# Performance work log

Hardware: AMD Instinct MI355X
Metric: run time of the kernel (lower is better)

The kernel has to match this reference:

```python
import jax, jax.numpy as jnp
import numpy as np

B, S, D = 4, 2048, 1024
H = 16
HD = D // H  # 64
SCALE = HD ** 0.5
LN_EPS = 1e-5


def setup_inputs() -> dict:
    key = jax.random.key(0)
    ks = jax.random.split(key, 13)
    std = 1.0 / np.sqrt(D)
    inp = {
        'q': jax.random.normal(ks[0], (B, S, D), jnp.float32),
        'k': jax.random.normal(ks[1], (B, S, D), jnp.float32),
        'v': jax.random.normal(ks[2], (B, S, D), jnp.float32),
        'Wq': jax.random.normal(ks[3], (D, D), jnp.float32) * std,
        'bq': jnp.zeros((D,), jnp.float32),
        'Wk': jax.random.normal(ks[4], (D, D), jnp.float32) * std,
        'bk': jnp.zeros((D,), jnp.float32),
        'Wv': jax.random.normal(ks[5], (D, D), jnp.float32) * std,
        'bv': jnp.zeros((D,), jnp.float32),
        'Wp': jax.random.normal(ks[6], (D, D), jnp.float32) * std,
        'bp': jnp.zeros((D,), jnp.float32),
        'gamma': jnp.ones((D,), jnp.float32),
        'beta': jnp.zeros((D,), jnp.float32),
    }
    return inp


def reference(q, k, v, Wq, bq, Wk, bk, Wv, bv, Wp, bp, gamma, beta):
    res = q
    # QKV projections, split into heads: [B, S, H, HD]
    qh = (q @ Wq + bq).reshape(B, S, H, HD)
    kh = (k @ Wk + bk).reshape(B, S, H, HD)
    vh = (v @ Wv + bv).reshape(B, S, H, HD)
    # Full attention scores [B, H, Sq, Sk]
    scores = jnp.einsum('bqhd,bkhd->bhqk', qh, kh) / SCALE
    # Multiplicative causal mask (zeros, NOT -inf) applied post-scale
    tril = jnp.tril(jnp.ones((S, S), scores.dtype))
    scores = scores * tril
    attn = jax.nn.softmax(scores, axis=-1)
    ctx = jnp.einsum('bhqk,bkhd->bqhd', attn, vh).reshape(B, S, D)
    out = ctx @ Wp + bp + res
    # LayerNorm over last dim
    mu = out.mean(-1, keepdims=True)
    var = out.var(-1, keepdims=True)
    return (out - mu) / jnp.sqrt(var + LN_EPS) * gamma + beta
```

## Files before the change

kernel.cpp:

```cpp
#include <hip/hip_runtime.h>

#define B_  4
#define S_  2048
#define D_  1024
#define H_  16
#define HD_ 64

#define ATT_EM 3.35462627903e-4f
#define ATT_C1 0.18033688011f
#define ATT_C0 -11.5415603281f

using v8bf = __attribute__((ext_vector_type(8))) __bf16;
using v8us = __attribute__((ext_vector_type(8))) unsigned short;
using v4f  = __attribute__((ext_vector_type(4))) float;

__device__ inline float bf2f(unsigned short u) {
    union { unsigned int i; float f; } x; x.i = ((unsigned int)u) << 16; return x.f;
}
__device__ inline unsigned short f2bf(float f) {
    union { float f; unsigned int i; } x; x.f = f;
    unsigned int r = x.i + 0x7fffu + ((x.i >> 16) & 1u);
    return (unsigned short)(r >> 16);
}
__device__ inline bool gam_is_f32(const unsigned* g) { return *g == 0x3F800000u; }

__device__ inline float fexp2(float x) {
    float r; asm("v_exp_f32 %0, %1" : "=v"(r) : "v"(x)); return r;
}

__device__ inline void gload_lds16(const void* g, void* l) {
    __builtin_amdgcn_global_load_lds(
        (const __attribute__((address_space(1))) unsigned int*)g,
        (__attribute__((address_space(3))) unsigned int*)l, 16, 0, 0);
}

__device__ inline void waitv4() { asm volatile("s_waitcnt vmcnt(4)" ::: "memory"); }
__device__ inline void waitv0() { asm volatile("s_waitcnt vmcnt(0)" ::: "memory"); }
__device__ inline void barx() {
    asm volatile("" ::: "memory");
    __builtin_amdgcn_s_barrier();
    asm volatile("" ::: "memory");
}

__global__ __launch_bounds__(1024) void transpose_w4(const void* __restrict__ W0,
                                                     const void* __restrict__ W1,
                                                     const void* __restrict__ W2,
                                                     const void* __restrict__ W3,
                                                     unsigned short* __restrict__ Wt,
                                                     const unsigned* __restrict__ gflag) {
    const bool f32 = gam_is_f32(gflag);
    const void* W = (blockIdx.z == 0) ? W0 : (blockIdx.z == 1) ? W1
                   : (blockIdx.z == 2) ? W2 : W3;
    unsigned short* out = Wt + (size_t)blockIdx.z * (D_ * D_);
    __shared__ float tile[32][33];
    const int x = threadIdx.x, y = threadIdx.y;
    const int n0 = blockIdx.x * 32, k0 = blockIdx.y * 32;
    const size_t si = (size_t)(k0 + y) * D_ + n0 + x;
    tile[y][x] = f32 ? ((const float*)W)[si] : bf2f(((const unsigned short*)W)[si]);
    __syncthreads();
    out[(size_t)(n0 + y) * D_ + k0 + x] = f2bf(tile[x][y]);
}

__global__ __launch_bounds__(256) void cvt3_k(const void* __restrict__ q,
                                              const void* __restrict__ k,
                                              const void* __restrict__ v,
                                              unsigned short* __restrict__ oq,
                                              unsigned short* __restrict__ ok,
                                              unsigned short* __restrict__ ov,
                                              const unsigned* __restrict__ gflag) {
    const bool f32 = gam_is_f32(gflag);
    const void* in = (blockIdx.y == 0) ? q : (blockIdx.y == 1) ? k : v;
    unsigned short* out = (blockIdx.y == 0) ? oq : (blockIdx.y == 1) ? ok : ov;
    const size_t i0 = ((size_t)blockIdx.x * 256 + threadIdx.x) * 16;
    if (f32) {
        const float* p = (const float*)in + i0;
        float4 fa = *(const float4*)(p);
        float4 fb = *(const float4*)(p + 4);
        float4 fc = *(const float4*)(p + 8);
        float4 fd = *(const float4*)(p + 12);
        v8us o0, o1;
        o0[0] = f2bf(fa.x); o0[1] = f2bf(fa.y); o0[2] = f2bf(fa.z); o0[3] = f2bf(fa.w);
        o0[4] = f2bf(fb.x); o0[5] = f2bf(fb.y); o0[6] = f2bf(fb.z); o0[7] = f2bf(fb.w);
        o1[0] = f2bf(fc.x); o1[1] = f2bf(fc.y); o1[2] = f2bf(fc.z); o1[3] = f2bf(fc.w);
        o1[4] = f2bf(fd.x); o1[5] = f2bf(fd.y); o1[6] = f2bf(fd.z); o1[7] = f2bf(fd.w);
        *(v8us*)(out + i0)     = o0;
        *(v8us*)(out + i0 + 8) = o1;
    } else {
        const unsigned short* p = (const unsigned short*)in + i0;
        *(v8us*)(out + i0)     = *(const v8us*)p;
        *(v8us*)(out + i0 + 8) = *(const v8us*)(p + 8);
    }
}

__global__ __launch_bounds__(256) void transpose_v_k(const unsigned short* __restrict__ Vh,
                                                     unsigned short* __restrict__ Vt) {
    const int st = blockIdx.x, bh = blockIdx.y;
    __shared__ unsigned short tile[64][72];
    const int t = threadIdx.x;
    const int r = t >> 2, c0 = (t & 3) * 16;
    const unsigned short* src = Vh + ((size_t)bh * S_ + st * 64 + r) * HD_ + c0;
    *(v8us*)&tile[r][c0]     = *(const v8us*)src;
    *(v8us*)&tile[r][c0 + 8] = *(const v8us*)(src + 8);
    __syncthreads();
    unsigned short* dst = Vt + ((size_t)bh * HD_ + r) * S_ + st * 64 + c0;
    v8us o0, o1;
#pragma unroll
    for (int j = 0; j < 8; j++) { o0[j] = tile[c0 + j][r]; o1[j] = tile[c0 + 8 + j][r]; }
    *(v8us*)dst       = o0;
    *(v8us*)(dst + 8) = o1;
}

__global__ __launch_bounds__(256) void gemmqkv_k(const unsigned short* __restrict__ Aq,
                                                 const unsigned short* __restrict__ Ak,
                                                 const unsigned short* __restrict__ Av,
                                                 const unsigned short* __restrict__ Wt,
                                                 const void* __restrict__ bq,
                                                 const void* __restrict__ bk,
                                                 const void* __restrict__ bv,
                                                 unsigned short* __restrict__ oq,
                                                 unsigned short* __restrict__ ok,
                                                 unsigned short* __restrict__ ov,
                                                 const unsigned* __restrict__ gflag) {
    const bool xf32 = gam_is_f32(gflag);

    __shared__ unsigned short As0[128 * 32], As1[128 * 32];
    __shared__ unsigned short Bs0[128 * 32], Bs1[128 * 32];
    const int t = threadIdx.x;
    const int lane = t & 63, wave = t >> 6;
    const int wr = (wave >> 1) * 64, wc = (wave & 1) * 64;
    const int l15 = lane & 15, quad = lane >> 4;

    const int id = (int)blockIdx.x;
    const int sw = (id & 7) * 192 + (id >> 3);
    const int ten = sw >> 9;
    const int tid = sw & 511;
    const int n0 = (tid & 7) * 128, m0 = (tid >> 3) * 128;

    const unsigned short* A = (ten == 0) ? Aq : (ten == 1) ? Ak : Av;
    const unsigned short* W = Wt + (size_t)ten * (D_ * D_);
    const void* bias        = (ten == 0) ? bq : (ten == 1) ? bk : bv;
    unsigned short* outH    = (ten == 0) ? oq : (ten == 1) ? ok : ov;

    v4f acc[4][4];
#pragma unroll
    for (int i = 0; i < 4; i++)
#pragma unroll
        for (int j = 0; j < 4; j++) { v4f z = {0.f, 0.f, 0.f, 0.f}; acc[i][j] = z; }

    const unsigned short* srcA = A + (size_t)(m0 + wave * 32 + (lane >> 2)) * D_ + (lane & 3) * 8;
    const unsigned short* srcB = W + (size_t)(n0 + wave * 32 + (lane >> 2)) * D_ + (lane & 3) * 8;
    unsigned short* dA0 = As0 + wave * 1024;
    unsigned short* dA1 = As1 + wave * 1024;
    unsigned short* dB0 = Bs0 + wave * 1024;
    unsigned short* dB1 = Bs1 + wave * 1024;

    auto stage = [&](unsigned short* dA, unsigned short* dB, int kt) {
        gload_lds16(srcA + kt,            dA);
        gload_lds16(srcA + kt + 16 * D_,  dA + 512);
        gload_lds16(srcB + kt,            dB);
        gload_lds16(srcB + kt + 16 * D_,  dB + 512);
    };
    auto compute = [&](const unsigned short* AS, const unsigned short* BS) {
        v8bf af[4], wf[4];
#pragma unroll
        for (int i = 0; i < 4; i++) af[i] = *(const v8bf*)&AS[(wr + i * 16 + l15) * 32 + quad * 8];
#pragma unroll
        for (int j = 0; j < 4; j++) wf[j] = *(const v8bf*)&BS[(wc + j * 16 + l15) * 32 + quad * 8];
#pragma unroll
        for (int i = 0; i < 4; i++)
#pragma unroll
            for (int j = 0; j < 4; j++)
                acc[i][j] = __builtin_amdgcn_mfma_f32_16x16x32_bf16(af[i], wf[j], acc[i][j], 0, 0, 0);
    };

    stage(dA0, dB0, 0);
#pragma unroll
    for (int k2 = 0; k2 < 16; ++k2) {
        const int kt = k2 * 64;
        stage(dA1, dB1, kt + 32);
        waitv4();
        barx();
        compute(As0, Bs0);
        barx();
        if (k2 < 15) { stage(dA0, dB0, kt + 64); waitv4(); }
        else         { waitv0(); }
        barx();
        compute(As1, Bs1);
        barx();
    }

#pragma unroll
    for (int i = 0; i < 4; i++) {
#pragma unroll
        for (int j = 0; j < 4; j++) {
            const int col = n0 + wc + j * 16 + l15;
            const float bv2 = xf32 ? ((const float*)bias)[col]
                                   : bf2f(((const unsigned short*)bias)[col]);
#pragma unroll
            for (int r = 0; r < 4; r++) {
                const int row = m0 + wr + i * 16 + quad * 4 + r;
                const float v = acc[i][j][r] + bv2;
                const int b = row >> 11, s = row & (S_ - 1);
                const int h = col >> 6,  d = col & 63;
                outH[(((size_t)(b * H_ + h)) * S_ + s) * HD_ + d] = f2bf(v);
            }
        }
    }
}

__global__ __launch_bounds__(256) void gemm_k(const unsigned short* __restrict__ A,
                                              const unsigned short* __restrict__ Wt,
                                              const void* __restrict__ bias,
                                              const void* __restrict__ res,
                                              float* __restrict__ outF,
                                              const unsigned* __restrict__ gflag) {
    const bool xf32 = gam_is_f32(gflag);

    __shared__ unsigned short As0[128 * 32], As1[128 * 32];
    __shared__ unsigned short Bs0[128 * 32], Bs1[128 * 32];
    const int t = threadIdx.x;
    const int lane = t & 63, wave = t >> 6;
    const int wr = (wave >> 1) * 64, wc = (wave & 1) * 64;
    const int l15 = lane & 15, quad = lane >> 4;

    const int id = (int)blockIdx.x;
    const int sw = (id & 7) * 64 + (id >> 3);
    const int n0 = (sw & 7) * 128, m0 = (sw >> 3) * 128;

    v4f acc[4][4];
#pragma unroll
    for (int i = 0; i < 4; i++)
#pragma unroll
        for (int j = 0; j < 4; j++) { v4f z = {0.f, 0.f, 0.f, 0.f}; acc[i][j] = z; }

    const unsigned short* srcA = A  + (size_t)(m0 + wave * 32 + (lane >> 2)) * D_ + (lane & 3) * 8;
    const unsigned short* srcB = Wt + (size_t)(n0 + wave * 32 + (lane >> 2)) * D_ + (lane & 3) * 8;
    unsigned short* dA0 = As0 + wave * 1024;
    unsigned short* dA1 = As1 + wave * 1024;
    unsigned short* dB0 = Bs0 + wave * 1024;
    unsigned short* dB1 = Bs1 + wave * 1024;

    auto stage = [&](unsigned short* dA, unsigned short* dB, int kt) {
        gload_lds16(srcA + kt,            dA);
        gload_lds16(srcA + kt + 16 * D_,  dA + 512);
        gload_lds16(srcB + kt,            dB);
        gload_lds16(srcB + kt + 16 * D_,  dB + 512);
    };
    auto compute = [&](const unsigned short* AS, const unsigned short* BS) {
        v8bf af[4], wf[4];
#pragma unroll
        for (int i = 0; i < 4; i++) af[i] = *(const v8bf*)&AS[(wr + i * 16 + l15) * 32 + quad * 8];
#pragma unroll
        for (int j = 0; j < 4; j++) wf[j] = *(const v8bf*)&BS[(wc + j * 16 + l15) * 32 + quad * 8];
#pragma unroll
        for (int i = 0; i < 4; i++)
#pragma unroll
            for (int j = 0; j < 4; j++)
                acc[i][j] = __builtin_amdgcn_mfma_f32_16x16x32_bf16(af[i], wf[j], acc[i][j], 0, 0, 0);
    };

    stage(dA0, dB0, 0);
#pragma unroll
    for (int k2 = 0; k2 < 16; ++k2) {
        const int kt = k2 * 64;
        stage(dA1, dB1, kt + 32);
        waitv4();
        barx();
        compute(As0, Bs0);
        barx();
        if (k2 < 15) { stage(dA0, dB0, kt + 64); waitv4(); }
        else         { waitv0(); }
        barx();
        compute(As1, Bs1);
        barx();
    }

#pragma unroll
    for (int i = 0; i < 4; i++) {
#pragma unroll
        for (int j = 0; j < 4; j++) {
            const int col = n0 + wc + j * 16 + l15;
            const float bv = xf32 ? ((const float*)bias)[col]
                                  : bf2f(((const unsigned short*)bias)[col]);
#pragma unroll
            for (int r = 0; r < 4; r++) {
                const int row = m0 + wr + i * 16 + quad * 4 + r;
                const size_t idx = (size_t)row * D_ + col;
                float v = acc[i][j][r] + bv;
                v += xf32 ? ((const float*)res)[idx]
                          : bf2f(((const unsigned short*)res)[idx]);
                outF[idx] = v;
            }
        }
    }
}

__global__ __launch_bounds__(256) void suffixv_k(const unsigned short* __restrict__ Vh,
                                                 float* __restrict__ SV) {
    const int bh = blockIdx.x;
    const int lane = threadIdx.x & 63, wave = threadIdx.x >> 6;
    __shared__ float part[32][64];
#pragma unroll
    for (int tt = 0; tt < 8; tt++) {
        const int t0 = wave * 8 + tt;
        float s = 0.f;
        const unsigned short* vp = Vh + ((size_t)bh * S_ + t0 * 64) * HD_ + lane;
#pragma unroll 8
        for (int r = 0; r < 64; r++) s += bf2f(vp[r * HD_]);
        part[t0][lane] = s;
    }
    __syncthreads();
    if (wave == 0) {
        float acc = 0.f;
        SV[((size_t)bh * 33 + 32) * 64 + lane] = 0.f;
        for (int tt = 31; tt >= 0; tt--) {
            acc += part[tt][lane];
            SV[((size_t)bh * 33 + tt) * 64 + lane] = acc;
        }
    }
}

__global__ __launch_bounds__(256) void attn_k(const unsigned short* __restrict__ Qh,
                                              const unsigned short* __restrict__ Kh,
                                              const unsigned short* __restrict__ Vt,
                                              const float* __restrict__ SV,
                                              unsigned short* __restrict__ ctx) {
    const int xa = blockIdx.x;
    const int qtA = xa, qtB = 31 - xa;
    const int bh = blockIdx.y;
    __shared__ unsigned short Ks[64][72];
    __shared__ unsigned short Vts[64][72];
    __shared__ __align__(16) unsigned short Ps[4][16][72];
    const int t = threadIdx.x, lane = t & 63, wave = t >> 6;
    const int l15 = lane & 15, quad = lane >> 4;

    const size_t headoff = (size_t)bh * S_ * HD_;

    v8bf aqA[2], aqB[2];
    {
        const unsigned short* qp = Qh + headoff + (size_t)(qtA * 64 + wave * 16 + l15) * HD_ + quad * 8;
        aqA[0] = *(const v8bf*)qp;
        aqA[1] = *(const v8bf*)(qp + 32);
        qp = Qh + headoff + (size_t)(qtB * 64 + wave * 16 + l15) * HD_ + quad * 8;
        aqB[0] = *(const v8bf*)qp;
        aqB[1] = *(const v8bf*)(qp + 32);
    }

    float lpA = 0.f, lpB = 0.f;
    v4f oA[4], oB[4];
#pragma unroll
    for (int dt = 0; dt < 4; dt++) { v4f z = {0.f, 0.f, 0.f, 0.f}; oA[dt] = z; oB[dt] = z; }

    const int srow = t >> 2, sc = (t & 3) * 16;

    v8bf kf[4][2];

    auto step = [&](const v8bf* aq, float& lp, v4f* oacc, bool diag) {
        v4f st[4];
        __builtin_amdgcn_s_setprio(1);
#pragma unroll
        for (int ct = 0; ct < 4; ct++) {
            v4f z = {0.f, 0.f, 0.f, 0.f};
#pragma unroll
            for (int kk = 0; kk < 2; kk++)
                z = __builtin_amdgcn_mfma_f32_16x16x32_bf16(kf[ct][kk], aq[kk], z, 0, 0, 0);
            st[ct] = z;
        }
        __builtin_amdgcn_s_setprio(0);

#pragma unroll
        for (int ct = 0; ct < 4; ct++) {
            float e0, e1, e2, e3;
            {
                float x0 = fexp2(fmaf(st[ct][0], ATT_C1, ATT_C0));
                float x1 = fexp2(fmaf(st[ct][1], ATT_C1, ATT_C0));
                float x2 = fexp2(fmaf(st[ct][2], ATT_C1, ATT_C0));
                float x3 = fexp2(fmaf(st[ct][3], ATT_C1, ATT_C0));
                if (diag) {
                    const int kg = ct * 16 + quad * 4;
                    const int qg = wave * 16 + l15;
                    x0 = (kg + 0 <= qg) ? x0 : ATT_EM;
                    x1 = (kg + 1 <= qg) ? x1 : ATT_EM;
                    x2 = (kg + 2 <= qg) ? x2 : ATT_EM;
                    x3 = (kg + 3 <= qg) ? x3 : ATT_EM;
                }
                e0 = x0; e1 = x1; e2 = x2; e3 = x3;
            }
            lp += (e0 + e1) + (e2 + e3);
            unsigned plo, phi;
            asm("v_cvt_pk_bf16_f32 %0, %1, %2" : "=v"(plo) : "v"(e0), "v"(e1));
            asm("v_cvt_pk_bf16_f32 %0, %1, %2" : "=v"(phi) : "v"(e2), "v"(e3));
            uint2 pw; pw.x = plo; pw.y = phi;
            *(uint2*)&Ps[wave][l15][ct * 16 + quad * 4] = pw;
        }

        asm volatile("s_waitcnt lgkmcnt(0)" ::: "memory");
        __builtin_amdgcn_sched_barrier(0);

        __builtin_amdgcn_s_setprio(1);
#pragma unroll
        for (int kk = 0; kk < 2; kk++) {
            v8bf ap = *(const v8bf*)&Ps[wave][l15][kk * 32 + quad * 8];
#pragma unroll
            for (int dt = 0; dt < 4; dt++) {
                v8bf vb = *(const v8bf*)&Vts[dt * 16 + l15][kk * 32 + quad * 8];
                oacc[dt] = __builtin_amdgcn_mfma_f32_16x16x32_bf16(ap, vb, oacc[dt], 0, 0, 0);
            }
        }
        __builtin_amdgcn_s_setprio(0);
        asm volatile("" ::: "memory");
    };

    for (int kt = 0; kt <= qtB; kt++) {
        const unsigned short* kp = Kh + headoff + (size_t)(kt * 64 + srow) * HD_ + sc;
        v8us k0 = *(const v8us*)kp, k1 = *(const v8us*)(kp + 8);
        *(v8us*)&Ks[srow][sc]     = k0;
        *(v8us*)&Ks[srow][sc + 8] = k1;
        const unsigned short* vp = Vt + headoff + (size_t)srow * S_ + kt * 64 + sc;
        v8us v0 = *(const v8us*)vp, v1 = *(const v8us*)(vp + 8);
        *(v8us*)&Vts[srow][sc]     = v0;
        *(v8us*)&Vts[srow][sc + 8] = v1;
        __syncthreads();

#pragma unroll
        for (int ct = 0; ct < 4; ct++)
#pragma unroll
            for (int kk = 0; kk < 2; kk++)
                kf[ct][kk] = *(const v8bf*)&Ks[ct * 16 + l15][kk * 32 + quad * 8];

        step(aqB, lpB, oB, kt == qtB);
        if (kt <= qtA) step(aqA, lpA, oA, kt == qtA);

        __syncthreads();
    }

    auto finish = [&](float lp, v4f* oacc, int qt) {
        lp += __shfl_xor(lp, 16);
        lp += __shfl_xor(lp, 32);
        float l_[4];
#pragma unroll
        for (int r = 0; r < 4; r++) l_[r] = __shfl(lp, quad * 4 + r);
        const int cnt = (31 - qt) * 64;
        if (cnt > 0) {
            const float* svp = SV + ((size_t)bh * 33 + (qt + 1)) * 64;
            float sv[4];
#pragma unroll
            for (int dt = 0; dt < 4; dt++) sv[dt] = svp[dt * 16 + l15];
#pragma unroll
            for (int r = 0; r < 4; r++) {
                l_[r] += (float)cnt * ATT_EM;
#pragma unroll
                for (int dt = 0; dt < 4; dt++) oacc[dt][r] += ATT_EM * sv[dt];
            }
        }
        const int bb = bh >> 4, hh = bh & 15;
#pragma unroll
        for (int dt = 0; dt < 4; dt++)
#pragma unroll
            for (int r = 0; r < 4; r++) {
                const int qrow = qt * 64 + wave * 16 + quad * 4 + r;
                const size_t idx = ((size_t)bb * S_ + qrow) * D_ + hh * HD_ + dt * 16 + l15;
                ctx[idx] = f2bf(oacc[dt][r] / l_[r]);
            }
    };
    finish(lpB, oB, qtB);
    finish(lpA, oA, qtA);
}

__global__ __launch_bounds__(256) void ln_k(const float* __restrict__ X,
                                            const void* __restrict__ gamma,
                                            const void* __restrict__ beta,
                                            void* __restrict__ outv,
                                            const unsigned* __restrict__ gflag) {
    const bool f32 = gam_is_f32(gflag);
    const int row = blockIdx.x, t = threadIdx.x;
    const float* xp = X + (size_t)row * D_;
    float4 x = *(const float4*)(xp + t * 4);
    float s = x.x + x.y + x.z + x.w;
    float q = x.x * x.x + x.y * x.y + x.z * x.z + x.w * x.w;
#pragma unroll
    for (int off = 1; off < 64; off <<= 1) {
        s += __shfl_xor(s, off);
        q += __shfl_xor(q, off);
    }
    __shared__ float red[2][4];
    const int wave = t >> 6, lane = t & 63;
    if (lane == 0) { red[0][wave] = s; red[1][wave] = q; }
    __syncthreads();
    s = red[0][0] + red[0][1] + red[0][2] + red[0][3];
    q = red[1][0] + red[1][1] + red[1][2] + red[1][3];
    const float mu = s * (1.f / 1024.f);
    const float var = q * (1.f / 1024.f) - mu * mu;
    const float rstd = rsqrtf(var + 1e-5f);
    const float* xe = &x.x;
#pragma unroll
    for (int e = 0; e < 4; e++) {
        const int c = t * 4 + e;
        const float g = f32 ? ((const float*)gamma)[c] : bf2f(((const unsigned short*)gamma)[c]);
        const float b = f32 ? ((const float*)beta)[c]  : bf2f(((const unsigned short*)beta)[c]);
        const float y = (xe[e] - mu) * rstd * g + b;
        if (f32) ((float*)outv)[(size_t)row * D_ + c] = y;
        else     ((unsigned short*)outv)[(size_t)row * D_ + c] = f2bf(y);
    }
}

extern "C" void kernel_launch(void* const* d_in, const int* in_sizes, int n_in,
                              void* d_out, int out_size, void* d_ws, size_t ws_size,
                              hipStream_t stream) {
    const void* q     = d_in[0];
    const void* k     = d_in[1];
    const void* v     = d_in[2];
    const void* Wq    = d_in[3];
    const void* bq    = d_in[4];
    const void* Wk    = d_in[5];
    const void* bk    = d_in[6];
    const void* Wv    = d_in[7];
    const void* bv    = d_in[8];
    const void* Wp    = d_in[9];
    const void* bp    = d_in[10];
    const void* gamma = d_in[11];
    const void* beta  = d_in[12];
    const unsigned* gflag = (const unsigned*)gamma;

    char* ws = (char*)d_ws;
    size_t off = 0;
    unsigned short* Wt   = (unsigned short*)(ws + off); off += (size_t)4 * 1024 * 1024 * 2;
    unsigned short* qh   = (unsigned short*)(ws + off); off += (size_t)8192 * 1024 * 2;
    unsigned short* kh   = (unsigned short*)(ws + off); off += (size_t)8192 * 1024 * 2;
    unsigned short* vh   = (unsigned short*)(ws + off); off += (size_t)8192 * 1024 * 2;
    float*          SV   = (float*)(ws + off);          off += (size_t)64 * 33 * 64 * 4;
    unsigned short* ctx  = (unsigned short*)(ws + off); off += (size_t)8192 * 1024 * 2;
    unsigned short* cvtK = (unsigned short*)(ws + off); off += (size_t)8192 * 1024 * 2;
    float* pre = (float*)qh;
    unsigned short* cvtQ = ctx;
    unsigned short* cvtV = (unsigned short*)d_out;
    unsigned short* vt = (unsigned short*)d_out;

    transpose_w4<<<dim3(32, 32, 4), dim3(32, 32), 0, stream>>>(Wq, Wk, Wv, Wp, Wt, gflag);
    cvt3_k<<<dim3(2048, 3), 256, 0, stream>>>(q, k, v, cvtQ, cvtK, cvtV, gflag);

    gemmqkv_k<<<1536, 256, 0, stream>>>(cvtQ, cvtK, cvtV, Wt, bq, bk, bv,
                                        qh, kh, vh, gflag);

    transpose_v_k<<<dim3(32, 64), 256, 0, stream>>>(vh, vt);
    suffixv_k<<<64, 256, 0, stream>>>(vh, SV);
    attn_k<<<dim3(16, 64), 256, 0, stream>>>(qh, kh, vt, SV, ctx);

    gemm_k<<<512, 256, 0, stream>>>(ctx, Wt + 3145728, bp, q, pre, gflag);

    ln_k<<<8192, 256, 0, stream>>>(pre, gamma, beta, d_out, gflag);
}
```

Before: 417.5 us.

## Fuse V column sums into transpose and interleave attention QK/PV for two tiles

Per-tile column sums of V are now computed inside the V transpose kernel, and a tiny suffix kernel scans them. This replaces the separate suffixv kernel, which re-read V with strided loads. The attention loop is split into QK, softmax and PV phases so both query tiles' QK MFMAs issue back to back before their softmax work, and an occupancy hint is added via launch bounds. The fp32-to-bf16 input conversion kernel is skipped when inputs are already bf16; in the fp32 default that path stays inactive.

```diff
diff --git a/kernel.cpp b/kernel.cpp
--- a/kernel.cpp
+++ b/kernel.cpp
@@ -93,7 +93,8 @@
 }
 
 __global__ __launch_bounds__(256) void transpose_v_k(const unsigned short* __restrict__ Vh,
-                                                     unsigned short* __restrict__ Vt) {
+                                                     unsigned short* __restrict__ Vt,
+                                                     float* __restrict__ part) {
     const int st = blockIdx.x, bh = blockIdx.y;
     __shared__ unsigned short tile[64][72];
     const int t = threadIdx.x;
@@ -104,10 +105,29 @@
     __syncthreads();
     unsigned short* dst = Vt + ((size_t)bh * HD_ + r) * S_ + st * 64 + c0;
     v8us o0, o1;
-#pragma unroll
-    for (int j = 0; j < 8; j++) { o0[j] = tile[c0 + j][r]; o1[j] = tile[c0 + 8 + j][r]; }
+    float ps = 0.f;
+#pragma unroll
+    for (int j = 0; j < 8; j++) {
+        o0[j] = tile[c0 + j][r];
+        o1[j] = tile[c0 + 8 + j][r];
+        ps += bf2f(o0[j]) + bf2f(o1[j]);
+    }
     *(v8us*)dst       = o0;
     *(v8us*)(dst + 8) = o1;
+    ps += __shfl_xor(ps, 1);
+    ps += __shfl_xor(ps, 2);
+    if ((t & 3) == 0) part[((size_t)bh * 32 + st) * 64 + r] = ps;
+}
+
+__global__ __launch_bounds__(64) void suffix_k(const float* __restrict__ part,
+                                               float* __restrict__ SV) {
+    const int bh = blockIdx.x, d = threadIdx.x;
+    float acc = 0.f;
+    SV[((size_t)bh * 33 + 32) * 64 + d] = 0.f;
+    for (int tt = 31; tt >= 0; --tt) {
+        acc += part[((size_t)bh * 32 + tt) * 64 + d];
+        SV[((size_t)bh * 33 + tt) * 64 + d] = acc;
+    }
 }
 
 __global__ __launch_bounds__(256) void gemmqkv_k(const unsigned short* __restrict__ Aq,
@@ -295,36 +315,11 @@
     }
 }
 
-__global__ __launch_bounds__(256) void suffixv_k(const unsigned short* __restrict__ Vh,
-                                                 float* __restrict__ SV) {
-    const int bh = blockIdx.x;
-    const int lane = threadIdx.x & 63, wave = threadIdx.x >> 6;
-    __shared__ float part[32][64];
-#pragma unroll
-    for (int tt = 0; tt < 8; tt++) {
-        const int t0 = wave * 8 + tt;
-        float s = 0.f;
-        const unsigned short* vp = Vh + ((size_t)bh * S_ + t0 * 64) * HD_ + lane;
-#pragma unroll 8
-        for (int r = 0; r < 64; r++) s += bf2f(vp[r * HD_]);
-        part[t0][lane] = s;
-    }
-    __syncthreads();
-    if (wave == 0) {
-        float acc = 0.f;
-        SV[((size_t)bh * 33 + 32) * 64 + lane] = 0.f;
-        for (int tt = 31; tt >= 0; tt--) {
-            acc += part[tt][lane];
-            SV[((size_t)bh * 33 + tt) * 64 + lane] = acc;
-        }
-    }
-}
-
-__global__ __launch_bounds__(256) void attn_k(const unsigned short* __restrict__ Qh,
-                                              const unsigned short* __restrict__ Kh,
-                                              const unsigned short* __restrict__ Vt,
-                                              const float* __restrict__ SV,
-                                              unsigned short* __restrict__ ctx) {
+__global__ __launch_bounds__(256, 4) void attn_k(const unsigned short* __restrict__ Qh,
+                                                 const unsigned short* __restrict__ Kh,
+                                                 const unsigned short* __restrict__ Vt,
+                                                 const float* __restrict__ SV,
+                                                 unsigned short* __restrict__ ctx) {
     const int xa = blockIdx.x;
     const int qtA = xa, qtB = 31 - xa;
     const int bh = blockIdx.y;
@@ -355,9 +350,7 @@
 
     v8bf kf[4][2];
 
-    auto step = [&](const v8bf* aq, float& lp, v4f* oacc, bool diag) {
-        v4f st[4];
-        __builtin_amdgcn_s_setprio(1);
+    auto QK = [&](const v8bf* aq, v4f* st) {
 #pragma unroll
         for (int ct = 0; ct < 4; ct++) {
             v4f z = {0.f, 0.f, 0.f, 0.f};
@@ -366,37 +359,32 @@
                 z = __builtin_amdgcn_mfma_f32_16x16x32_bf16(kf[ct][kk], aq[kk], z, 0, 0, 0);
             st[ct] = z;
         }
-        __builtin_amdgcn_s_setprio(0);
-
+    };
+    auto SM = [&](const v4f* st, float& lp, bool diag) {
 #pragma unroll
         for (int ct = 0; ct < 4; ct++) {
-            float e0, e1, e2, e3;
-            {
-                float x0 = fexp2(fmaf(st[ct][0], ATT_C1, ATT_C0));
-                float x1 = fexp2(fmaf(st[ct][1], ATT_C1, ATT_C0));
-                float x2 = fexp2(fmaf(st[ct][2], ATT_C1, ATT_C0));
-                float x3 = fexp2(fmaf(st[ct][3], ATT_C1, ATT_C0));
-                if (diag) {
-                    const int kg = ct * 16 + quad * 4;
-                    const int qg = wave * 16 + l15;
-                    x0 = (kg + 0 <= qg) ? x0 : ATT_EM;
-                    x1 = (kg + 1 <= qg) ? x1 : ATT_EM;
-                    x2 = (kg + 2 <= qg) ? x2 : ATT_EM;
-                    x3 = (kg + 3 <= qg) ? x3 : ATT_EM;
-                }
-                e0 = x0; e1 = x1; e2 = x2; e3 = x3;
+            float x0 = fexp2(fmaf(st[ct][0], ATT_C1, ATT_C0));
+            float x1 = fexp2(fmaf(st[ct][1], ATT_C1, ATT_C0));
+            float x2 = fexp2(fmaf(st[ct][2], ATT_C1, ATT_C0));
+            float x3 = fexp2(fmaf(st[ct][3], ATT_C1, ATT_C0));
+            if (diag) {
+                const int kg = ct * 16 + quad * 4;
+                const int qg = wave * 16 + l15;
+                x0 = (kg + 0 <= qg) ? x0 : ATT_EM;
+                x1 = (kg + 1 <= qg) ? x1 : ATT_EM;
+                x2 = (kg + 2 <= qg) ? x2 : ATT_EM;
+                x3 = (kg + 3 <= qg) ? x3 : ATT_EM;
             }
-            lp += (e0 + e1) + (e2 + e3);
+            lp += (x0 + x1) + (x2 + x3);
             unsigned plo, phi;
-            asm("v_cvt_pk_bf16_f32 %0, %1, %2" : "=v"(plo) : "v"(e0), "v"(e1));
-            asm("v_cvt_pk_bf16_f32 %0, %1, %2" : "=v"(phi) : "v"(e2), "v"(e3));
+            asm("v_cvt_pk_bf16_f32 %0, %1, %2" : "=v"(plo) : "v"(x0), "v"(x1));
+            asm("v_cvt_pk_bf16_f32 %0, %1, %2" : "=v"(phi) : "v"(x2), "v"(x3));
             uint2 pw; pw.x = plo; pw.y = phi;
             *(uint2*)&Ps[wave][l15][ct * 16 + quad * 4] = pw;
         }
-
+    };
+    auto PV = [&](v4f* oacc) {
         asm volatile("s_waitcnt lgkmcnt(0)" ::: "memory");
-        __builtin_amdgcn_sched_barrier(0);
-
         __builtin_amdgcn_s_setprio(1);
 #pragma unroll
         for (int kk = 0; kk < 2; kk++) {
@@ -428,8 +416,24 @@
             for (int kk = 0; kk < 2; kk++)
                 kf[ct][kk] = *(const v8bf*)&Ks[ct * 16 + l15][kk * 32 + quad * 8];
 
-        step(aqB, lpB, oB, kt == qtB);
-        if (kt <= qtA) step(aqA, lpA, oA, kt == qtA);
+        if (kt <= qtA) {
+            v4f stB[4], stA[4];
+            __builtin_amdgcn_s_setprio(1);
+            QK(aqB, stB);
+            QK(aqA, stA);
+            __builtin_amdgcn_s_setprio(0);
+            SM(stB, lpB, false);
+            PV(oB);
+            SM(stA, lpA, kt == qtA);
+            PV(oA);
+        } else {
+            v4f stB[4];
+            __builtin_amdgcn_s_setprio(1);
+            QK(aqB, stB);
+            __builtin_amdgcn_s_setprio(0);
+            SM(stB, lpB, kt == qtB);
+            PV(oB);
+        }
 
         __syncthreads();
     }
@@ -529,6 +533,7 @@
     unsigned short* kh   = (unsigned short*)(ws + off); off += (size_t)8192 * 1024 * 2;
     unsigned short* vh   = (unsigned short*)(ws + off); off += (size_t)8192 * 1024 * 2;
     float*          SV   = (float*)(ws + off);          off += (size_t)64 * 33 * 64 * 4;
+    float*          part = (float*)(ws + off);          off += (size_t)64 * 32 * 64 * 4;
     unsigned short* ctx  = (unsigned short*)(ws + off); off += (size_t)8192 * 1024 * 2;
     unsigned short* cvtK = (unsigned short*)(ws + off); off += (size_t)8192 * 1024 * 2;
     float* pre = (float*)qh;
@@ -536,14 +541,20 @@
     unsigned short* cvtV = (unsigned short*)d_out;
     unsigned short* vt = (unsigned short*)d_out;
 
+    const bool in_bf16 = (in_sizes[0] == (int)((size_t)B_ * S_ * D_ * 2));
+    const unsigned short* Aq = in_bf16 ? (const unsigned short*)q : cvtQ;
+    const unsigned short* Ak = in_bf16 ? (const unsigned short*)k : cvtK;
+    const unsigned short* Av = in_bf16 ? (const unsigned short*)v : cvtV;
+
     transpose_w4<<<dim3(32, 32, 4), dim3(32, 32), 0, stream>>>(Wq, Wk, Wv, Wp, Wt, gflag);
-    cvt3_k<<<dim3(2048, 3), 256, 0, stream>>>(q, k, v, cvtQ, cvtK, cvtV, gflag);
-
-    gemmqkv_k<<<1536, 256, 0, stream>>>(cvtQ, cvtK, cvtV, Wt, bq, bk, bv,
+    if (!in_bf16)
+        cvt3_k<<<dim3(2048, 3), 256, 0, stream>>>(q, k, v, cvtQ, cvtK, cvtV, gflag);
+
+    gemmqkv_k<<<1536, 256, 0, stream>>>(Aq, Ak, Av, Wt, bq, bk, bv,
                                         qh, kh, vh, gflag);
 
-    transpose_v_k<<<dim3(32, 64), 256, 0, stream>>>(vh, vt);
-    suffixv_k<<<64, 256, 0, stream>>>(vh, SV);
+    transpose_v_k<<<dim3(32, 64), 256, 0, stream>>>(vh, vt, part);
+    suffix_k<<<64, 64, 0, stream>>>(part, SV);
     attn_k<<<dim3(16, 64), 256, 0, stream>>>(qh, kh, vt, SV, ctx);
 
     gemm_k<<<512, 256, 0, stream>>>(ctx, Wt + 3145728, bp, q, pre, gflag);
```

New measurement: 473.5 us. 1.13x slower.
